# Performance work log

Measured on AMD Instinct MI355X. Metric: run time of the kernel, lower is better.

The kernel has to match this reference:

```python
import jax, jax.numpy as jnp
import numpy as np

B, S, D = 4, 2048, 1024
HEADS, KEY_SIZE, SIZE_PER_HEAD = 16, 64, 64
OUT_DIM = HEADS * SIZE_PER_HEAD
NEG_BIG = 1e10


def setup_inputs() -> dict:
    key = jax.random.key(0)
    ks = jax.random.split(key, 6)
    q_value = jax.random.normal(ks[0], (B, S, D), dtype=jnp.float32)
    k_value = jax.random.normal(ks[1], (B, S, D), dtype=jnp.float32)
    v_value = jax.random.normal(ks[2], (B, S, D), dtype=jnp.float32)
    v_mask = jnp.ones((B, S, 1), dtype=jnp.float32)
    q_mask = jnp.ones((B, S, 1), dtype=jnp.float32)
    scale = 1.0 / np.sqrt(D)
    Wq = jax.random.normal(ks[3], (D, HEADS * KEY_SIZE), dtype=jnp.float32) * scale
    Wk = jax.random.normal(ks[4], (D, HEADS * KEY_SIZE), dtype=jnp.float32) * scale
    Wv = jax.random.normal(ks[5], (D, OUT_DIM), dtype=jnp.float32) * scale
    return {"q_value": q_value, "k_value": k_value, "v_value": v_value,
            "v_mask": v_mask, "q_mask": q_mask, "Wq": Wq, "Wk": Wk, "Wv": Wv}


def reference(q_value, k_value, v_value, v_mask, q_mask, Wq, Wk, Wv):
    b, sq, _ = q_value.shape
    sk = k_value.shape[1]
    # projections (no bias) -> [B, S, H, dh]
    qw = (q_value @ Wq).reshape(b, sq, HEADS, KEY_SIZE)
    kw = (k_value @ Wk).reshape(b, sk, HEADS, KEY_SIZE)
    vw = (v_value @ Wv).reshape(b, sk, HEADS, SIZE_PER_HEAD)
    # scores [B, H, Sq, Sk], scaled by sqrt(key_size)
    scores = jnp.einsum('bqhd,bkhd->bhqk', qw, kw) / jnp.sqrt(
        jnp.asarray(KEY_SIZE, dtype=qw.dtype))
    # additive key-side mask: v_mask [B, Sk, 1] -> broadcast over heads/queries
    scores = scores - (1.0 - v_mask[:, None, None, :, 0]) * NEG_BIG
    attn = jax.nn.softmax(scores, axis=-1)
    out = jnp.einsum('bhqk,bkhd->bqhd', attn, vw).reshape(b, sq, OUT_DIM)
    # multiplicative query-side mask
    return out * q_mask
```

## Files before the change

### kernel.cpp

```cpp
#include <hip/hip_runtime.h>

typedef __bf16 bf16_t;
typedef __bf16 bf16x8 __attribute__((ext_vector_type(8)));
typedef __bf16 bf16x4 __attribute__((ext_vector_type(4)));
typedef __bf16 bf16x2 __attribute__((ext_vector_type(2)));
typedef float  f32x4  __attribute__((ext_vector_type(4)));
typedef float  f32x16 __attribute__((ext_vector_type(16)));
typedef unsigned int u32x4 __attribute__((ext_vector_type(4)));
typedef int i32x2 __attribute__((ext_vector_type(2)));

#define MFMA16(A, B, C) __builtin_amdgcn_mfma_f32_16x16x32_bf16((A), (B), (C), 0, 0, 0)
#define MFMA32(A, B, C) __builtin_amdgcn_mfma_f32_32x32x16_bf16((A), (B), (C), 0, 0, 0)

constexpr int BB = 4;
constexpr int SS = 2048;
constexpr int DD = 1024;
constexpr int HH = 16;
constexpr int DH = 64;
constexpr float C1 = 0.18033688011112042f;
constexpr float C2 = 1.4426950408889634e10f;

__device__ __forceinline__ void async_copy16(const void* g, void* l) {
    __builtin_amdgcn_global_load_lds(
        (const __attribute__((address_space(1))) void*)g,
        (__attribute__((address_space(3))) void*)l, 16, 0, 0);
}

__device__ __forceinline__ unsigned pack_bf16(float lo, float hi) {
    bf16x2 t;
    t[0] = (bf16_t)lo;
    t[1] = (bf16_t)hi;
    return __builtin_bit_cast(unsigned, t);
}

__device__ __forceinline__ void permswap(unsigned& a, unsigned& b) {
    i32x2 r = __builtin_amdgcn_permlane32_swap((int)a, (int)b, false, false);
    a = (unsigned)r[0];
    b = (unsigned)r[1];
}

__device__ __forceinline__ void packP(const f32x16& st, bf16x8& w0, bf16x8& w1) {
    unsigned a0 = pack_bf16(st[0],  st[1]);
    unsigned a1 = pack_bf16(st[2],  st[3]);
    unsigned a2 = pack_bf16(st[4],  st[5]);
    unsigned a3 = pack_bf16(st[6],  st[7]);
    unsigned a4 = pack_bf16(st[8],  st[9]);
    unsigned a5 = pack_bf16(st[10], st[11]);
    unsigned a6 = pack_bf16(st[12], st[13]);
    unsigned a7 = pack_bf16(st[14], st[15]);
    permswap(a0, a2);
    permswap(a1, a3);
    permswap(a4, a6);
    permswap(a5, a7);
    u32x4 u0 = {a0, a1, a2, a3};
    u32x4 u1 = {a4, a5, a6, a7};
    w0 = __builtin_bit_cast(bf16x8, u0);
    w1 = __builtin_bit_cast(bf16x8, u1);
}

__global__ __launch_bounds__(256) void conv_kernel(
    const float* __restrict__ q, const float* __restrict__ k,
    const float* __restrict__ v, bf16_t* __restrict__ outb)
{
    const float* src = blockIdx.z == 0 ? q : blockIdx.z == 1 ? k : v;
    bf16_t* dst = outb + ((size_t)blockIdx.z << 23);
    size_t i = ((size_t)blockIdx.x * 256 + threadIdx.x) * 8;
    f32x4 a = *(const f32x4*)&src[i];
    f32x4 b = *(const f32x4*)&src[i + 4];
    bf16x8 o;
    o[0] = (bf16_t)a[0]; o[1] = (bf16_t)a[1]; o[2] = (bf16_t)a[2]; o[3] = (bf16_t)a[3];
    o[4] = (bf16_t)b[0]; o[5] = (bf16_t)b[1]; o[6] = (bf16_t)b[2]; o[7] = (bf16_t)b[3];
    *(bf16x8*)&dst[i] = o;
}

__global__ __launch_bounds__(256) void wtrans_kernel(
    const float* __restrict__ Wq, const float* __restrict__ Wk,
    const float* __restrict__ Wv, bf16_t* __restrict__ Wt)
{
    const float* W = blockIdx.z == 0 ? Wq : blockIdx.z == 1 ? Wk : Wv;
    bf16_t* T = Wt + ((size_t)blockIdx.z << 20);

    __shared__ __align__(16) bf16_t tile[64][72];

    const int k0 = blockIdx.x * 64;
    const int n0 = blockIdx.y * 64;
    const int tid = threadIdx.x;

    #pragma unroll
    for (int i = 0; i < 4; i++) {
        int idx = tid + i * 256;
        int kk = idx >> 4;
        int nn = (idx & 15) * 4;
        f32x4 w = *(const f32x4*)&W[(size_t)(k0 + kk) * 1024 + n0 + nn];
        tile[nn + 0][kk] = (bf16_t)w[0];
        tile[nn + 1][kk] = (bf16_t)w[1];
        tile[nn + 2][kk] = (bf16_t)w[2];
        tile[nn + 3][kk] = (bf16_t)w[3];
    }
    __syncthreads();
    #pragma unroll
    for (int i = 0; i < 2; i++) {
        int idx = tid + i * 256;
        int nn = idx >> 3;
        int kk = (idx & 7) * 8;
        *(bf16x8*)&T[(size_t)(n0 + nn) * 1024 + k0 + kk] =
            *(const bf16x8*)&tile[nn][kk];
    }
}

__global__ __launch_bounds__(256) void proj_kernel(
    const bf16_t* __restrict__ Ab, const bf16_t* __restrict__ Wt,
    bf16_t* __restrict__ qw, bf16_t* __restrict__ kw, bf16_t* __restrict__ vwt)
{
    const int which = blockIdx.z;
    const bf16_t* A = Ab + ((size_t)which << 23);
    const bf16_t* T = Wt + ((size_t)which << 20);

    __shared__ bf16_t Alds[128 * 64];
    __shared__ bf16_t Blds[128 * 64];

    const int tid = threadIdx.x;
    const int lane = tid & 63;
    const int wave = tid >> 6;
    const int quad = lane >> 4;
    const int l16 = lane & 15;

    const int id = blockIdx.x;
    const int xg = id & 7;
    const int sl = id >> 3;
    const int m0 = (((xg << 3) | (sl >> 3))) * 128;
    const int n0 = (sl & 7) * 128;

    const int wm = (wave >> 1) * 64;
    const int wn = (wave & 1) * 64;

    const int srow = lane >> 3;
    const int schk = lane & 7;

    f32x4 zero4 = {0.f, 0.f, 0.f, 0.f};
    f32x4 acc[4][4];
    #pragma unroll
    for (int i = 0; i < 4; i++)
        #pragma unroll
        for (int j = 0; j < 4; j++) acc[i][j] = zero4;

    for (int k0 = 0; k0 < DD; k0 += 64) {
        #pragma unroll
        for (int j = 0; j < 4; j++) {
            int r0 = wave * 32 + j * 8;
            int row = r0 + srow;
            int c = schk ^ (row & 7);
            async_copy16(&A[(size_t)(m0 + row) * 1024 + k0 + c * 8], &Alds[r0 * 64]);
        }
        #pragma unroll
        for (int j = 0; j < 4; j++) {
            int r0 = wave * 32 + j * 8;
            int row = r0 + srow;
            int c = schk ^ (row & 7);
            async_copy16(&T[(size_t)(n0 + row) * 1024 + k0 + c * 8], &Blds[r0 * 64]);
        }
        __syncthreads();

        #pragma unroll
        for (int s = 0; s < 2; s++) {
            bf16x8 af[4], bfr[4];
            #pragma unroll
            for (int mi = 0; mi < 4; mi++)
                af[mi] = *(const bf16x8*)&Alds[(wm + mi * 16 + l16) * 64 +
                             (((s * 4 + quad) ^ (l16 & 7)) << 3)];
            #pragma unroll
            for (int ni = 0; ni < 4; ni++)
                bfr[ni] = *(const bf16x8*)&Blds[(wn + ni * 16 + l16) * 64 +
                              (((s * 4 + quad) ^ (l16 & 7)) << 3)];
            #pragma unroll
            for (int mi = 0; mi < 4; mi++)
                #pragma unroll
                for (int ni = 0; ni < 4; ni++)
                    acc[mi][ni] = MFMA16(af[mi], bfr[ni], acc[mi][ni]);
        }
        __syncthreads();
    }

    if (which < 2) {
        bf16_t* Cout = which == 0 ? qw : kw;
        #pragma unroll
        for (int mi = 0; mi < 4; mi++)
            #pragma unroll
            for (int ni = 0; ni < 4; ni++)
                #pragma unroll
                for (int r = 0; r < 4; r++) {
                    int row = m0 + wm + mi * 16 + quad * 4 + r;
                    int col = n0 + wn + ni * 16 + l16;
                    Cout[(size_t)row * 1024 + col] = (bf16_t)acc[mi][ni][r];
                }
    } else {
        #pragma unroll
        for (int mi = 0; mi < 4; mi++)
            #pragma unroll
            for (int ni = 0; ni < 4; ni++) {
                int s0 = m0 + wm + mi * 16 + quad * 4;
                int col = n0 + wn + ni * 16 + l16;
                int b = s0 >> 11, s = s0 & 2047;
                int h = col >> 6, d = col & 63;
                bf16x4 p;
                p[0] = (bf16_t)acc[mi][ni][0]; p[1] = (bf16_t)acc[mi][ni][1];
                p[2] = (bf16_t)acc[mi][ni][2]; p[3] = (bf16_t)acc[mi][ni][3];
                *(bf16x4*)&vwt[(((size_t)((b * HH + h) * DH + d)) << 11) + s] = p;
            }
    }
}

__global__ __launch_bounds__(256) void attn_kernel(
    const bf16_t* __restrict__ qw, const bf16_t* __restrict__ kw,
    const bf16_t* __restrict__ vwt, const float* __restrict__ v_mask,
    const float* __restrict__ q_mask, float* __restrict__ out)
{
    const int linear = blockIdx.x;
    const int xg = linear & 7;
    const int sl = linear >> 3;
    const int grp = (xg << 3) | (sl >> 4);
    const int qt = sl & 15;
    const int b = grp >> 4;
    const int h = grp & 15;

    __shared__ __align__(16) bf16_t KV[4 * 4096];
    __shared__ float lred[2][2][64];

    const int tid = threadIdx.x;
    const int lane = tid & 63;
    const int wave = tid >> 6;
    const int qg = wave >> 1;
    const int kh = wave & 1;
    const int l5 = lane & 31;
    const int hi = lane >> 5;
    const int q0 = qt * 128 + qg * 64;

    const int srow = lane >> 3;
    const int schk = lane & 7;
    const int ck = schk ^ srow;

    bf16x8 qf[2][4];
    #pragma unroll
    for (int qb = 0; qb < 2; ++qb)
        #pragma unroll
        for (int c = 0; c < 4; ++c)
            qf[qb][c] = *(const bf16x8*)&qw[(size_t)(b * SS + q0 + qb * 32 + l5) * 1024 +
                                            h * 64 + c * 16 + hi * 8];

    f32x16 zero16;
    #pragma unroll
    for (int i = 0; i < 16; ++i) zero16[i] = 0.f;

    const int vkh = (l5 & 7) ^ hi;
    const bf16_t* pk[4];
    #pragma unroll
    for (int c = 0; c < 4; ++c)
        pk[c] = &KV[kh * 2048 + l5 * 64 + ((vkh ^ (2 * c)) << 3)];
    const bf16_t* pv[2];
    #pragma unroll
    for (int ks = 0; ks < 2; ++ks)
        pv[ks] = &KV[8192 + l5 * 64 + ((vkh ^ (4 * kh) ^ (2 * ks)) << 3)];

    const bf16_t* gk = &kw[(size_t)(b * SS + wave * 16 + srow) * 1024 + h * 64 + ck * 8];
    const bf16_t* gv = &vwt[(((size_t)((b * HH + h) * DH + wave * 16 + srow)) << 11) +
                            ck * 8];
    const float* pvm = v_mask + b * SS + kh * 32 + hi * 4;

    auto stage = [&](int bi) {
        #pragma unroll
        for (int j = 0; j < 2; ++j)
            async_copy16(gk + j * 8192, &KV[bi * 4096 + (wave * 16 + j * 8) * 64]);
        gk += 64 * 1024;
        #pragma unroll
        for (int j = 0; j < 2; ++j)
            async_copy16(gv + j * 16384, &KV[8192 + bi * 4096 + (wave * 16 + j * 8) * 64]);
        gv += 64;
    };

    stage(0);
    __syncthreads();

    f32x16 o00 = zero16, o01 = zero16, o10 = zero16, o11 = zero16;
    f32x4 la = {0.f, 0.f, 0.f, 0.f};
    f32x4 lb = {0.f, 0.f, 0.f, 0.f};

    for (int t2 = 0; t2 < 32; t2 += 2) {
        #pragma unroll
        for (int cur = 0; cur < 2; ++cur) {
            const int t = t2 + cur;

            f32x4 vm4[4];
            #pragma unroll
            for (int g = 0; g < 4; ++g)
                vm4[g] = *(const f32x4*)(pvm + g * 8);
            pvm += 64;

            if (t < 31) stage(cur ^ 1);

            __builtin_amdgcn_s_setprio(1);
            f32x16 st0, st1;
            {
                bf16x8 kf = *(const bf16x8*)(pk[0] + cur * 4096);
                st0 = MFMA32(kf, qf[0][0], zero16);
                st1 = MFMA32(kf, qf[1][0], zero16);
            }
            #pragma unroll
            for (int c = 1; c < 4; ++c) {
                bf16x8 kf = *(const bf16x8*)(pk[c] + cur * 4096);
                st0 = MFMA32(kf, qf[0][c], st0);
                st1 = MFMA32(kf, qf[1][c], st1);
            }
            __builtin_amdgcn_s_setprio(0);

            #pragma unroll
            for (int g = 0; g < 4; ++g) {
                #pragma unroll
                for (int j = 0; j < 4; ++j) {
                    float nv = __builtin_fmaf(vm4[g][j], C2, -C2);
                    float p0 = __builtin_amdgcn_exp2f(
                        __builtin_fmaf(st0[g * 4 + j], C1, nv));
                    st0[g * 4 + j] = p0;
                    la[j] += p0;
                    float p1 = __builtin_amdgcn_exp2f(
                        __builtin_fmaf(st1[g * 4 + j], C1, nv));
                    st1[g * 4 + j] = p1;
                    lb[j] += p1;
                }
            }

            bf16x8 bp00, bp01, bp10, bp11;
            packP(st0, bp00, bp01);
            packP(st1, bp10, bp11);

            __builtin_amdgcn_s_setprio(1);
            #pragma unroll
            for (int ks = 0; ks < 2; ++ks) {
                bf16x8 bpa = ks ? bp01 : bp00;
                bf16x8 bpb = ks ? bp11 : bp10;
                bf16x8 av0 = *(const bf16x8*)(pv[ks] + cur * 4096);
                bf16x8 av1 = *(const bf16x8*)(pv[ks] + cur * 4096 + 2048);
                o00 = MFMA32(av0, bpa, o00);
                o10 = MFMA32(av0, bpb, o10);
                o01 = MFMA32(av1, bpa, o01);
                o11 = MFMA32(av1, bpb, o11);
            }
            __builtin_amdgcn_s_setprio(0);

            __syncthreads();
        }
    }

    float ls0 = (la[0] + la[1]) + (la[2] + la[3]);
    float ls1 = (lb[0] + lb[1]) + (lb[2] + lb[3]);
    float* R = (float*)KV;

    if (kh == 1) {
        *(f32x16*)&R[((qg * 2 + 0) * 2 + 0) * 1024 + lane * 16] = o00;
        *(f32x16*)&R[((qg * 2 + 0) * 2 + 1) * 1024 + lane * 16] = o01;
        *(f32x16*)&R[((qg * 2 + 1) * 2 + 0) * 1024 + lane * 16] = o10;
        *(f32x16*)&R[((qg * 2 + 1) * 2 + 1) * 1024 + lane * 16] = o11;
        lred[qg][0][lane] = ls0;
        lred[qg][1][lane] = ls1;
    }
    __syncthreads();
    if (kh == 0) {
        o00 += *(const f32x16*)&R[((qg * 2 + 0) * 2 + 0) * 1024 + lane * 16];
        o01 += *(const f32x16*)&R[((qg * 2 + 0) * 2 + 1) * 1024 + lane * 16];
        o10 += *(const f32x16*)&R[((qg * 2 + 1) * 2 + 0) * 1024 + lane * 16];
        o11 += *(const f32x16*)&R[((qg * 2 + 1) * 2 + 1) * 1024 + lane * 16];
        ls0 += lred[qg][0][lane];
        ls1 += lred[qg][1][lane];
        ls0 += __shfl_xor(ls0, 32);
        ls1 += __shfl_xor(ls1, 32);

        const float sc0 = q_mask[b * SS + q0 + l5] / ls0;
        const float sc1 = q_mask[b * SS + q0 + 32 + l5] / ls1;

        #pragma unroll
        for (int qb = 0; qb < 2; ++qb) {
            const float sc = qb ? sc1 : sc0;
            const int q = q0 + qb * 32 + l5;
            #pragma unroll
            for (int db = 0; db < 2; ++db) {
                const f32x16 oa = qb ? (db ? o11 : o10) : (db ? o01 : o00);
                #pragma unroll
                for (int g = 0; g < 4; ++g) {
                    f32x4 o4;
                    o4[0] = oa[g * 4 + 0] * sc;
                    o4[1] = oa[g * 4 + 1] * sc;
                    o4[2] = oa[g * 4 + 2] * sc;
                    o4[3] = oa[g * 4 + 3] * sc;
                    *(f32x4*)&out[(size_t)(b * SS + q) * 1024 + h * 64 +
                                  db * 32 + g * 8 + hi * 4] = o4;
                }
            }
        }
    }
}

extern "C" void kernel_launch(void* const* d_in, const int* in_sizes, int n_in,
                              void* d_out, int out_size, void* d_ws, size_t ws_size,
                              hipStream_t stream)
{
    const float* q  = (const float*)d_in[0];
    const float* k  = (const float*)d_in[1];
    const float* v  = (const float*)d_in[2];
    const float* vm = (const float*)d_in[3];
    const float* qm = (const float*)d_in[4];
    const float* Wq = (const float*)d_in[5];
    const float* Wk = (const float*)d_in[6];
    const float* Wv = (const float*)d_in[7];
    float* out = (float*)d_out;

    const size_t elems = (size_t)BB * SS * DD;
    bf16_t* Ab  = (bf16_t*)d_ws;
    bf16_t* qw  = Ab + 3 * elems;
    bf16_t* kw  = qw + elems;
    bf16_t* vwt = kw + elems;
    bf16_t* Wt  = vwt + elems;

    conv_kernel<<<dim3(4096, 1, 3), 256, 0, stream>>>(q, k, v, Ab);
    wtrans_kernel<<<dim3(16, 16, 3), 256, 0, stream>>>(Wq, Wk, Wv, Wt);
    proj_kernel<<<dim3(512, 1, 3), 256, 0, stream>>>(Ab, Wt, qw, kw, vwt);
    attn_kernel<<<dim3(1024, 1, 1), 256, 0, stream>>>(qw, kw, vwt, vm, qm, out);
}
```

Baseline: 328.3 us.

## Give each attention wave private K/V staging to drop per-tile block barriers

Restructures the attention kernel into 2-wave blocks (one query group of 64, two key halves), where each wave loads its own K/V slice through registers into a private double-buffered shared-memory region. This removes the __syncthreads after every key tile and replaces the async global-to-LDS copies with register-staged loads written between compute phases. The grid doubles to 2048 blocks of 128 threads. In exchange, each wave re-reads K/V that were previously shared across two query groups, so global traffic rises, and the extra staging registers may lower occupancy.

```diff
diff --git a/kernel.cpp b/kernel.cpp
--- a/kernel.cpp
+++ b/kernel.cpp
@@ -210,7 +210,7 @@
     }
 }
 
-__global__ __launch_bounds__(256) void attn_kernel(
+__global__ __launch_bounds__(128) void attn_kernel(
     const bf16_t* __restrict__ qw, const bf16_t* __restrict__ kw,
     const bf16_t* __restrict__ vwt, const float* __restrict__ v_mask,
     const float* __restrict__ q_mask, float* __restrict__ out)
@@ -218,26 +218,22 @@
     const int linear = blockIdx.x;
     const int xg = linear & 7;
     const int sl = linear >> 3;
-    const int grp = (xg << 3) | (sl >> 4);
-    const int qt = sl & 15;
+    const int grp = (xg << 3) | (sl >> 5);
+    const int qt = sl & 31;
     const int b = grp >> 4;
     const int h = grp & 15;
 
-    __shared__ __align__(16) bf16_t KV[4 * 4096];
-    __shared__ float lred[2][2][64];
+    __shared__ __align__(16) bf16_t KV[2 * 8192];
+    __shared__ float lred[2][64];
 
     const int tid = threadIdx.x;
     const int lane = tid & 63;
-    const int wave = tid >> 6;
-    const int qg = wave >> 1;
-    const int kh = wave & 1;
+    const int kh = tid >> 6;
     const int l5 = lane & 31;
     const int hi = lane >> 5;
-    const int q0 = qt * 128 + qg * 64;
-
-    const int srow = lane >> 3;
-    const int schk = lane & 7;
-    const int ck = schk ^ srow;
+    const int q0 = qt * 64;
+
+    bf16_t* W = &KV[kh * 8192];
 
     bf16x8 qf[2][4];
     #pragma unroll
@@ -255,30 +251,45 @@
     const bf16_t* pk[4];
     #pragma unroll
     for (int c = 0; c < 4; ++c)
-        pk[c] = &KV[kh * 2048 + l5 * 64 + ((vkh ^ (2 * c)) << 3)];
+        pk[c] = &W[l5 * 64 + ((vkh ^ (2 * c)) << 3)];
     const bf16_t* pv[2];
     #pragma unroll
     for (int ks = 0; ks < 2; ++ks)
-        pv[ks] = &KV[8192 + l5 * 64 + ((vkh ^ (4 * kh) ^ (2 * ks)) << 3)];
-
-    const bf16_t* gk = &kw[(size_t)(b * SS + wave * 16 + srow) * 1024 + h * 64 + ck * 8];
-    const bf16_t* gv = &vwt[(((size_t)((b * HH + h) * DH + wave * 16 + srow)) << 11) +
-                            ck * 8];
+        pv[ks] = &W[4096 + l5 * 32 + (((ks * 2 + hi) ^ (l5 & 3)) << 3)];
+
+    const bf16_t* gk = &kw[(size_t)(b * SS + kh * 32 + (lane >> 3)) * 1024 +
+                           h * 64 + (lane & 7) * 8];
+    const bf16_t* gv = &vwt[(((size_t)((b * HH + h) * DH + (lane >> 2))) << 11) +
+                            kh * 32 + (lane & 3) * 8];
     const float* pvm = v_mask + b * SS + kh * 32 + hi * 4;
-
-    auto stage = [&](int bi) {
-        #pragma unroll
-        for (int j = 0; j < 2; ++j)
-            async_copy16(gk + j * 8192, &KV[bi * 4096 + (wave * 16 + j * 8) * 64]);
-        gk += 64 * 1024;
-        #pragma unroll
-        for (int j = 0; j < 2; ++j)
-            async_copy16(gv + j * 16384, &KV[8192 + bi * 4096 + (wave * 16 + j * 8) * 64]);
-        gv += 64;
+    bf16_t* wk = &W[(lane >> 3) * 64 + (((lane & 7) ^ (lane >> 3)) << 3)];
+    bf16_t* wv = &W[4096 + (lane >> 2) * 32 + (((lane & 3) ^ ((lane >> 2) & 3)) << 3)];
+
+    u32x4 sk[4], sv[4];
+    auto load_kv = [&](int t) {
+        const bf16_t* k0p = gk + (size_t)t * 65536;
+        #pragma unroll
+        for (int j = 0; j < 4; ++j)
+            sk[j] = *(const u32x4*)(k0p + j * 8192);
+        const bf16_t* v0p = gv + t * 64;
+        #pragma unroll
+        for (int j = 0; j < 4; ++j)
+            sv[j] = *(const u32x4*)(v0p + j * 32768);
     };
-
-    stage(0);
-    __syncthreads();
+    auto write_k = [&](int buf) {
+        #pragma unroll
+        for (int j = 0; j < 4; ++j)
+            *(u32x4*)(wk + buf * 2048 + j * 512) = sk[j];
+    };
+    auto write_v = [&](int buf) {
+        #pragma unroll
+        for (int j = 0; j < 4; ++j)
+            *(u32x4*)(wv + buf * 2048 + j * 512) = sv[j];
+    };
+
+    load_kv(0);
+    write_k(0);
+    write_v(0);
 
     f32x16 o00 = zero16, o01 = zero16, o10 = zero16, o11 = zero16;
     f32x4 la = {0.f, 0.f, 0.f, 0.f};
@@ -288,6 +299,8 @@
         #pragma unroll
         for (int cur = 0; cur < 2; ++cur) {
             const int t = t2 + cur;
+            const bool pre = t < 31;
+            const int cb = cur * 2048;
 
             f32x4 vm4[4];
             #pragma unroll
@@ -295,22 +308,24 @@
                 vm4[g] = *(const f32x4*)(pvm + g * 8);
             pvm += 64;
 
-            if (t < 31) stage(cur ^ 1);
+            if (pre) load_kv(t + 1);
 
             __builtin_amdgcn_s_setprio(1);
             f32x16 st0, st1;
             {
-                bf16x8 kf = *(const bf16x8*)(pk[0] + cur * 4096);
+                bf16x8 kf = *(const bf16x8*)(pk[0] + cb);
                 st0 = MFMA32(kf, qf[0][0], zero16);
                 st1 = MFMA32(kf, qf[1][0], zero16);
             }
             #pragma unroll
             for (int c = 1; c < 4; ++c) {
-                bf16x8 kf = *(const bf16x8*)(pk[c] + cur * 4096);
+                bf16x8 kf = *(const bf16x8*)(pk[c] + cb);
                 st0 = MFMA32(kf, qf[0][c], st0);
                 st1 = MFMA32(kf, qf[1][c], st1);
             }
             __builtin_amdgcn_s_setprio(0);
+
+            if (pre) write_k(cur ^ 1);
 
             #pragma unroll
             for (int g = 0; g < 4; ++g) {
@@ -337,8 +352,8 @@
             for (int ks = 0; ks < 2; ++ks) {
                 bf16x8 bpa = ks ? bp01 : bp00;
                 bf16x8 bpb = ks ? bp11 : bp10;
-                bf16x8 av0 = *(const bf16x8*)(pv[ks] + cur * 4096);
-                bf16x8 av1 = *(const bf16x8*)(pv[ks] + cur * 4096 + 2048);
+                bf16x8 av0 = *(const bf16x8*)(pv[ks] + cb);
+                bf16x8 av1 = *(const bf16x8*)(pv[ks] + cb + 1024);
                 o00 = MFMA32(av0, bpa, o00);
                 o10 = MFMA32(av0, bpb, o10);
                 o01 = MFMA32(av1, bpa, o01);
@@ -346,30 +361,30 @@
             }
             __builtin_amdgcn_s_setprio(0);
 
-            __syncthreads();
+            if (pre) write_v(cur ^ 1);
         }
     }
 
     float ls0 = (la[0] + la[1]) + (la[2] + la[3]);
     float ls1 = (lb[0] + lb[1]) + (lb[2] + lb[3]);
-    float* R = (float*)KV;
+    float* R = (float*)&KV[8192];
 
     if (kh == 1) {
-        *(f32x16*)&R[((qg * 2 + 0) * 2 + 0) * 1024 + lane * 16] = o00;
-        *(f32x16*)&R[((qg * 2 + 0) * 2 + 1) * 1024 + lane * 16] = o01;
-        *(f32x16*)&R[((qg * 2 + 1) * 2 + 0) * 1024 + lane * 16] = o10;
-        *(f32x16*)&R[((qg * 2 + 1) * 2 + 1) * 1024 + lane * 16] = o11;
-        lred[qg][0][lane] = ls0;
-        lred[qg][1][lane] = ls1;
+        *(f32x16*)&R[0 * 1024 + lane * 16] = o00;
+        *(f32x16*)&R[1 * 1024 + lane * 16] = o01;
+        *(f32x16*)&R[2 * 1024 + lane * 16] = o10;
+        *(f32x16*)&R[3 * 1024 + lane * 16] = o11;
+        lred[0][lane] = ls0;
+        lred[1][lane] = ls1;
     }
     __syncthreads();
     if (kh == 0) {
-        o00 += *(const f32x16*)&R[((qg * 2 + 0) * 2 + 0) * 1024 + lane * 16];
-        o01 += *(const f32x16*)&R[((qg * 2 + 0) * 2 + 1) * 1024 + lane * 16];
-        o10 += *(const f32x16*)&R[((qg * 2 + 1) * 2 + 0) * 1024 + lane * 16];
-        o11 += *(const f32x16*)&R[((qg * 2 + 1) * 2 + 1) * 1024 + lane * 16];
-        ls0 += lred[qg][0][lane];
-        ls1 += lred[qg][1][lane];
+        o00 += *(const f32x16*)&R[0 * 1024 + lane * 16];
+        o01 += *(const f32x16*)&R[1 * 1024 + lane * 16];
+        o10 += *(const f32x16*)&R[2 * 1024 + lane * 16];
+        o11 += *(const f32x16*)&R[3 * 1024 + lane * 16];
+        ls0 += lred[0][lane];
+        ls1 += lred[1][lane];
         ls0 += __shfl_xor(ls0, 32);
         ls1 += __shfl_xor(ls1, 32);
 
@@ -422,5 +437,5 @@
     conv_kernel<<<dim3(4096, 1, 3), 256, 0, stream>>>(q, k, v, Ab);
     wtrans_kernel<<<dim3(16, 16, 3), 256, 0, stream>>>(Wq, Wk, Wv, Wt);
     proj_kernel<<<dim3(512, 1, 3), 256, 0, stream>>>(Ab, Wt, qw, kw, vwt);
-    attn_kernel<<<dim3(1024, 1, 1), 256, 0, stream>>>(qw, kw, vwt, vm, qm, out);
-}
+    attn_kernel<<<dim3(2048, 1, 1), 128, 0, stream>>>(qw, kw, vwt, vm, qm, out);
+}
```

Result: slower. 356.2 us (+8.5%).

## Split K and V staging into separate phases with vmcnt-guarded barriers

Applied to the files above, without the earlier changes.

Tile staging is split into a K phase and a V phase. Each phase issues its async global-to-LDS loads for the next buffer and then synchronises with an explicit s_waitcnt vmcnt plus s_barrier, replacing the single __syncthreads at the end of each iteration. The key mask is now copied into LDS with the same async loads instead of being read from global memory in every iteration. The aim is to let V loads overlap the QK and softmax work and to shorten barrier stalls. The cost is two barriers per tile and correctness that depends on hand-counted outstanding-load counts.

```diff
diff --git a/kernel.cpp b/kernel.cpp
--- a/kernel.cpp
+++ b/kernel.cpp
@@ -25,6 +25,17 @@
         (const __attribute__((address_space(1))) void*)g,
         (__attribute__((address_space(3))) void*)l, 16, 0, 0);
 }
+__device__ __forceinline__ void async_copy4(const void* g, void* l) {
+    __builtin_amdgcn_global_load_lds(
+        (const __attribute__((address_space(1))) void*)g,
+        (__attribute__((address_space(3))) void*)l, 4, 0, 0);
+}
+
+#define PHASE_SYNC(N) do {                                          \
+    asm volatile("s_waitcnt vmcnt(" #N ")" ::: "memory");           \
+    __builtin_amdgcn_s_barrier();                                   \
+    __builtin_amdgcn_sched_barrier(0);                              \
+} while (0)
 
 __device__ __forceinline__ unsigned pack_bf16(float lo, float hi) {
     bf16x2 t;
@@ -224,6 +235,7 @@
     const int h = grp & 15;
 
     __shared__ __align__(16) bf16_t KV[4 * 4096];
+    __shared__ float vml[2][64];
     __shared__ float lred[2][2][64];
 
     const int tid = threadIdx.x;
@@ -260,25 +272,26 @@
     #pragma unroll
     for (int ks = 0; ks < 2; ++ks)
         pv[ks] = &KV[8192 + l5 * 64 + ((vkh ^ (4 * kh) ^ (2 * ks)) << 3)];
+    const float* vmlp = &vml[0][kh * 32 + hi * 4];
 
     const bf16_t* gk = &kw[(size_t)(b * SS + wave * 16 + srow) * 1024 + h * 64 + ck * 8];
     const bf16_t* gv = &vwt[(((size_t)((b * HH + h) * DH + wave * 16 + srow)) << 11) +
                             ck * 8];
-    const float* pvm = v_mask + b * SS + kh * 32 + hi * 4;
-
-    auto stage = [&](int bi) {
-        #pragma unroll
-        for (int j = 0; j < 2; ++j)
-            async_copy16(gk + j * 8192, &KV[bi * 4096 + (wave * 16 + j * 8) * 64]);
-        gk += 64 * 1024;
-        #pragma unroll
-        for (int j = 0; j < 2; ++j)
-            async_copy16(gv + j * 16384, &KV[8192 + bi * 4096 + (wave * 16 + j * 8) * 64]);
-        gv += 64;
+    const float* vsrc = v_mask + b * SS + lane;
+
+    auto stageK = [&](int bi) {
+        async_copy16(gk,        &KV[bi * 4096 + (wave * 16) * 64]);
+        async_copy16(gk + 8192, &KV[bi * 4096 + (wave * 16 + 8) * 64]);
+        async_copy4(vsrc, &vml[bi][0]);
     };
-
-    stage(0);
-    __syncthreads();
+    auto stageV = [&](int bi) {
+        async_copy16(gv,         &KV[8192 + bi * 4096 + (wave * 16) * 64]);
+        async_copy16(gv + 16384, &KV[8192 + bi * 4096 + (wave * 16 + 8) * 64]);
+    };
+
+    stageK(0);
+    stageV(0);
+    gk += 65536; gv += 64; vsrc += 64;
 
     f32x16 o00 = zero16, o01 = zero16, o10 = zero16, o11 = zero16;
     f32x4 la = {0.f, 0.f, 0.f, 0.f};
@@ -287,26 +300,23 @@
     for (int t2 = 0; t2 < 32; t2 += 2) {
         #pragma unroll
         for (int cur = 0; cur < 2; ++cur) {
-            const int t = t2 + cur;
-
-            f32x4 vm4[4];
-            #pragma unroll
-            for (int g = 0; g < 4; ++g)
-                vm4[g] = *(const f32x4*)(pvm + g * 8);
-            pvm += 64;
-
-            if (t < 31) stage(cur ^ 1);
+            const int cb = cur * 4096;
+            const bool adv = (t2 + cur) < 30;
+
+            stageK(cur ^ 1);
+            if (adv) { gk += 65536; vsrc += 64; }
+            PHASE_SYNC(5);
 
             __builtin_amdgcn_s_setprio(1);
             f32x16 st0, st1;
             {
-                bf16x8 kf = *(const bf16x8*)(pk[0] + cur * 4096);
+                bf16x8 kf = *(const bf16x8*)(pk[0] + cb);
                 st0 = MFMA32(kf, qf[0][0], zero16);
                 st1 = MFMA32(kf, qf[1][0], zero16);
             }
             #pragma unroll
             for (int c = 1; c < 4; ++c) {
-                bf16x8 kf = *(const bf16x8*)(pk[c] + cur * 4096);
+                bf16x8 kf = *(const bf16x8*)(pk[c] + cb);
                 st0 = MFMA32(kf, qf[0][c], st0);
                 st1 = MFMA32(kf, qf[1][c], st1);
             }
@@ -314,9 +324,10 @@
 
             #pragma unroll
             for (int g = 0; g < 4; ++g) {
+                f32x4 vm4 = *(const f32x4*)(vmlp + cur * 64 + g * 8);
                 #pragma unroll
                 for (int j = 0; j < 4; ++j) {
-                    float nv = __builtin_fmaf(vm4[g][j], C2, -C2);
+                    float nv = __builtin_fmaf(vm4[j], C2, -C2);
                     float p0 = __builtin_amdgcn_exp2f(
                         __builtin_fmaf(st0[g * 4 + j], C1, nv));
                     st0[g * 4 + j] = p0;
@@ -332,23 +343,28 @@
             packP(st0, bp00, bp01);
             packP(st1, bp10, bp11);
 
+            stageV(cur ^ 1);
+            if (adv) gv += 64;
+            PHASE_SYNC(5);
+
             __builtin_amdgcn_s_setprio(1);
             #pragma unroll
             for (int ks = 0; ks < 2; ++ks) {
                 bf16x8 bpa = ks ? bp01 : bp00;
                 bf16x8 bpb = ks ? bp11 : bp10;
-                bf16x8 av0 = *(const bf16x8*)(pv[ks] + cur * 4096);
-                bf16x8 av1 = *(const bf16x8*)(pv[ks] + cur * 4096 + 2048);
+                bf16x8 av0 = *(const bf16x8*)(pv[ks] + cb);
+                bf16x8 av1 = *(const bf16x8*)(pv[ks] + cb + 2048);
                 o00 = MFMA32(av0, bpa, o00);
                 o10 = MFMA32(av0, bpb, o10);
                 o01 = MFMA32(av1, bpa, o01);
                 o11 = MFMA32(av1, bpb, o11);
             }
             __builtin_amdgcn_s_setprio(0);
-
-            __syncthreads();
         }
     }
+
+    asm volatile("s_waitcnt vmcnt(0)" ::: "memory");
+    __syncthreads();
 
     float ls0 = (la[0] + la[1]) + (la[2] + la[3]);
     float ls1 = (lb[0] + lb[1]) + (lb[2] + lb[3]);
```

Result: slower. 378.0 us (+15.2%).
